# Optimization experiments

Measured on AMD Instinct MI355X. Metric: run time of the kernel, lower is better.

Reference implementation:

```python
import jax, jax.numpy as jnp
import numpy as np
import math

N_EMBD = 1024
N_HEAD = 16
B, T = 2, 2048
MASK_VAL = -10.0  # non-standard soft mask value from original module


def setup_inputs() -> dict:
    key = jax.random.key(0)
    k1, k2, k3 = jax.random.split(key, 3)
    scale = 1.0 / math.sqrt(N_EMBD)
    x = jax.random.normal(k1, (B, T, N_EMBD), dtype=jnp.float32)
    # torch Linear weights: (out_features, in_features)
    w_attn = jax.random.normal(k2, (3 * N_EMBD, N_EMBD), dtype=jnp.float32) * scale
    w_proj = jax.random.normal(k3, (N_EMBD, N_EMBD), dtype=jnp.float32) * scale
    return {"x": x, "w_attn": w_attn, "w_proj": w_proj}


def reference(x, w_attn, w_proj):
    Bsz, Tlen, C = x.shape
    hs = C // N_HEAD
    qkv = jnp.einsum('btc,fc->btf', x, w_attn)  # [B,T,3C]
    q, k, v = jnp.split(qkv, 3, axis=-1)
    # [B,H,T,hs]
    q = q.reshape(Bsz, Tlen, N_HEAD, hs).transpose(0, 2, 1, 3)
    k = k.reshape(Bsz, Tlen, N_HEAD, hs).transpose(0, 2, 1, 3)
    v = v.reshape(Bsz, Tlen, N_HEAD, hs).transpose(0, 2, 1, 3)
    att = jnp.einsum('bhqd,bhkd->bhqk', q, k) * (1.0 / math.sqrt(hs))
    causal = jnp.tril(jnp.ones((Tlen, Tlen), dtype=bool))
    att = jnp.where(causal[None, None], att, MASK_VAL)
    att = jax.nn.softmax(att, axis=-1)
    y = jnp.einsum('bhqk,bhkd->bhqd', att, v)
    y = y.transpose(0, 2, 1, 3).reshape(Bsz, Tlen, C)
    return jnp.einsum('btc,fc->btf', y, w_proj)
```

## Files before the change

### kernel.cpp

```cpp
#include <hip/hip_runtime.h>
#include <hip/hip_bf16.h>
#include <stdint.h>

#define BSZ   2
#define TT    2048
#define NH    16
#define HS    64
#define CC    1024
#define C3    3072
#define MT    4096
#define E10   4.5399929762484854e-05f
#define SCL2  0.1803368801111204f

typedef __bf16 bf16;
typedef __bf16 bf16x8 __attribute__((ext_vector_type(8)));
typedef float  f32x4  __attribute__((ext_vector_type(4)));
typedef short  s16x4  __attribute__((ext_vector_type(4)));

#define AS1 __attribute__((address_space(1)))
#define AS3 __attribute__((address_space(3)))

__device__ __forceinline__ void glds16(const bf16* g, bf16* l) {
    __builtin_amdgcn_global_load_lds((const AS1 void*)g, (AS3 void*)l, 16, 0, 0);
}

__global__ void detect_dtype(const uint16_t* __restrict__ x, int* __restrict__ flag) {
    __shared__ int cnt;
    if (threadIdx.x == 0) cnt = 0;
    __syncthreads();
    int local = 0;
    for (int i = threadIdx.x; i < 512; i += 256) {
        uint16_t u = x[i];
        int e = (u >> 7) & 0xFF;
        if (e >= 96 && e <= 159) local++;
    }
    atomicAdd(&cnt, local);
    __syncthreads();
    if (threadIdx.x == 0) *flag = (cnt >= 461) ? 0 : 1;
}

#define NX8  (MT * CC / 8)
#define NWA8 (C3 * CC / 8)
#define NWP8 (CC * CC / 8)
__global__ __launch_bounds__(256)
void convert_all(const float* __restrict__ x, const float* __restrict__ wa,
                 const float* __restrict__ wp, bf16* __restrict__ xd,
                 bf16* __restrict__ wad, bf16* __restrict__ wpd,
                 const int* __restrict__ flag) {
    if (*flag == 0) return;
    long i = (long)blockIdx.x * 256 + threadIdx.x;
    const float* s; bf16* d; long off;
    if (i < NX8)             { s = x;  d = xd;  off = i; }
    else if (i < NX8 + NWA8) { s = wa; d = wad; off = i - NX8; }
    else                     { s = wp; d = wpd; off = i - NX8 - NWA8; }
    const float4* sp = reinterpret_cast<const float4*>(s) + off * 2;
    float4 a = sp[0], b = sp[1];
    bf16x8 r;
    r[0] = (bf16)a.x; r[1] = (bf16)a.y; r[2] = (bf16)a.z; r[3] = (bf16)a.w;
    r[4] = (bf16)b.x; r[5] = (bf16)b.y; r[6] = (bf16)b.z; r[7] = (bf16)b.w;
    reinterpret_cast<bf16x8*>(d)[off] = r;
}

__global__ __launch_bounds__(256)
void gemm_bt(const bf16* __restrict__ A0, const bf16* __restrict__ A1,
             const bf16* __restrict__ B0, const bf16* __restrict__ B1,
             void* __restrict__ Cmain, bf16* __restrict__ Cv,
             const int* __restrict__ flag,
             int M, int N, int K, int lda, int ldb, int ldc,
             int split_col, int cf32_dyn) {
    __shared__ bf16 As[2][128 * 32];
    __shared__ bf16 Bs[2][128 * 32];

    const int f = *flag;
    const bf16* A = f ? A1 : A0;
    const bf16* B = f ? B1 : B0;
    const int cf32 = cf32_dyn & f;

    const int tid  = threadIdx.x;
    const int lane = tid & 63;
    const int wave = tid >> 6;
    const int wm   = wave >> 1;
    const int wn   = wave & 1;
    const int quad = lane >> 4;
    const int l16  = lane & 15;

    const int row0 = blockIdx.y * 128;
    const int col0 = blockIdx.x * 128;

    const int srow = tid >> 2;
    const int skk  = (tid & 3) * 8;

    const bf16* Ap = A + (long)(row0 + srow) * lda + skk;
    const bf16* Bp = B + (long)(col0 + srow) * ldb + skk;

    auto stage = [&](int k0, int buf) {
        glds16(Ap + k0,                  &As[buf][wave * 512]);
        glds16(Ap + (long)64 * lda + k0, &As[buf][wave * 512 + 2048]);
        glds16(Bp + k0,                  &Bs[buf][wave * 512]);
        glds16(Bp + (long)64 * ldb + k0, &Bs[buf][wave * 512 + 2048]);
    };

    f32x4 acc[4][4] = {};
    stage(0, 0);

    for (int k0 = 0; k0 < K; k0 += 32) {
        const int buf = (k0 >> 5) & 1;
        __syncthreads();
        if (k0 + 32 < K) stage(k0 + 32, buf ^ 1);

        const bf16* Ac = As[buf];
        const bf16* Bc = Bs[buf];
        bf16x8 af[4], bfv[4];
#pragma unroll
        for (int mi = 0; mi < 4; ++mi)
            af[mi] = *reinterpret_cast<const bf16x8*>(&Ac[(wm * 64 + mi * 16 + l16) * 32 + quad * 8]);
#pragma unroll
        for (int ni = 0; ni < 4; ++ni)
            bfv[ni] = *reinterpret_cast<const bf16x8*>(&Bc[(wn * 64 + ni * 16 + l16) * 32 + quad * 8]);
#pragma unroll
        for (int mi = 0; mi < 4; ++mi)
#pragma unroll
            for (int ni = 0; ni < 4; ++ni)
                acc[mi][ni] = __builtin_amdgcn_mfma_f32_16x16x32_bf16(af[mi], bfv[ni], acc[mi][ni], 0, 0, 0);
    }

    if (split_col < 0 || col0 < split_col) {
#pragma unroll
        for (int mi = 0; mi < 4; ++mi)
#pragma unroll
            for (int ni = 0; ni < 4; ++ni)
#pragma unroll
                for (int r = 0; r < 4; ++r) {
                    int row = row0 + wm * 64 + mi * 16 + quad * 4 + r;
                    int col = col0 + wn * 64 + ni * 16 + l16;
                    float v = acc[mi][ni][r];
                    if (cf32) ((float*)Cmain)[(long)row * ldc + col] = v;
                    else      ((bf16*)Cmain)[(long)row * ldc + col] = (bf16)v;
                }
    } else {
        const int h  = (col0 - split_col + wn * 64) >> 6;
        const int bq = row0 >> 11;
        const int tc = ((row0 & 2047) >> 6) + wm;
#pragma unroll
        for (int ni = 0; ni < 4; ++ni) {
            long vrow = (long)(bq * NH + h) * 64 + ni * 16 + l16;
#pragma unroll
            for (int mi = 0; mi < 4; ++mi) {
                bf16 outv[4];
#pragma unroll
                for (int r = 0; r < 4; ++r) outv[r] = (bf16)acc[mi][ni][r];
                *reinterpret_cast<uint2*>(&Cv[vrow * 2048 + tc * 64 + quad * 16 + mi * 4]) =
                    *reinterpret_cast<uint2*>(outv);
            }
        }
    }
}

__global__ __launch_bounds__(256)
void gemm_bt64(const bf16* __restrict__ A0, const bf16* __restrict__ A1,
               const bf16* __restrict__ B0, const bf16* __restrict__ B1,
               void* __restrict__ C, const int* __restrict__ flag,
               int M, int N, int K, int lda, int ldb, int ldc, int cf32_dyn) {
    __shared__ bf16 As[2][128 * 32];
    __shared__ bf16 Bs[2][64 * 32];

    const int f = *flag;
    const bf16* A = f ? A1 : A0;
    const bf16* B = f ? B1 : B0;
    const int cf32 = cf32_dyn & f;

    const int tid  = threadIdx.x;
    const int lane = tid & 63;
    const int wave = tid >> 6;
    const int wm   = wave >> 1;
    const int wn   = wave & 1;
    const int quad = lane >> 4;
    const int l16  = lane & 15;

    const int row0 = blockIdx.y * 128;
    const int col0 = blockIdx.x * 64;

    const int srow = tid >> 2;
    const int skk  = (tid & 3) * 8;

    const bf16* Ap = A + (long)(row0 + srow) * lda + skk;
    const bf16* Bp = B + (long)(col0 + srow) * ldb + skk;

    auto stage = [&](int k0, int buf) {
        glds16(Ap + k0,                  &As[buf][wave * 512]);
        glds16(Ap + (long)64 * lda + k0, &As[buf][wave * 512 + 2048]);
        glds16(Bp + k0,                  &Bs[buf][wave * 512]);
    };

    f32x4 acc[4][2] = {};
    stage(0, 0);

    for (int k0 = 0; k0 < K; k0 += 32) {
        const int buf = (k0 >> 5) & 1;
        __syncthreads();
        if (k0 + 32 < K) stage(k0 + 32, buf ^ 1);

        const bf16* Ac = As[buf];
        const bf16* Bc = Bs[buf];
        bf16x8 af[4], bfv[2];
#pragma unroll
        for (int mi = 0; mi < 4; ++mi)
            af[mi] = *reinterpret_cast<const bf16x8*>(&Ac[(wm * 64 + mi * 16 + l16) * 32 + quad * 8]);
#pragma unroll
        for (int ni = 0; ni < 2; ++ni)
            bfv[ni] = *reinterpret_cast<const bf16x8*>(&Bc[(wn * 32 + ni * 16 + l16) * 32 + quad * 8]);
#pragma unroll
        for (int mi = 0; mi < 4; ++mi)
#pragma unroll
            for (int ni = 0; ni < 2; ++ni)
                acc[mi][ni] = __builtin_amdgcn_mfma_f32_16x16x32_bf16(af[mi], bfv[ni], acc[mi][ni], 0, 0, 0);
    }

#pragma unroll
    for (int mi = 0; mi < 4; ++mi)
#pragma unroll
        for (int ni = 0; ni < 2; ++ni)
#pragma unroll
            for (int r = 0; r < 4; ++r) {
                int row = row0 + wm * 64 + mi * 16 + quad * 4 + r;
                int col = col0 + wn * 32 + ni * 16 + l16;
                float v = acc[mi][ni][r];
                if (cf32) ((float*)C)[(long)row * ldc + col] = v;
                else      ((bf16*)C)[(long)row * ldc + col] = (bf16)v;
            }
}

__global__ __launch_bounds__(256)
void vtile2(const bf16* __restrict__ Vt, float* __restrict__ Vtile) {
    const int kt = blockIdx.x, bh = blockIdx.y;
    const int tid = threadIdx.x;
    const int d = tid >> 2, part = tid & 3;
    const bf16* p = Vt + ((long)bh * 64 + d) * 2048 + kt * 64 + part * 16;
    float s = 0.f;
#pragma unroll
    for (int i = 0; i < 2; ++i) {
        bf16x8 v = *reinterpret_cast<const bf16x8*>(p + i * 8);
#pragma unroll
        for (int j = 0; j < 8; ++j) s += (float)v[j];
    }
    s += __shfl_xor(s, 1, 64);
    s += __shfl_xor(s, 2, 64);
    if (part == 0) Vtile[((long)bh * 32 + kt) * 64 + d] = s;
}

__global__ void vts_suffix(const float* __restrict__ Vtile, float* __restrict__ Vts) {
    const int bh = blockIdx.x, d = threadIdx.x;
    Vts[((long)bh * 33 + 32) * 64 + d] = 0.f;
    float acc = 0.f;
    for (int kt = 31; kt >= 0; --kt) {
        acc += Vtile[((long)bh * 32 + kt) * 64 + d];
        Vts[((long)bh * 33 + kt) * 64 + d] = acc;
    }
}

__global__ __launch_bounds__(256, 3)
void attn(bf16* __restrict__ qk, const bf16* __restrict__ Vt,
          const float* __restrict__ Vts) {
    __shared__ bf16 Ks[3][64 * 64];
    __shared__ bf16 Vs[3][64 * 64];

    const int tid  = threadIdx.x;
    const int lane = tid & 63;
    const int wave = tid >> 6;
    const int quad = lane >> 4;
    const int l16  = lane & 15;

    const int f2   = blockIdx.x;
    const int xcd  = f2 & 7;
    const int slot = f2 >> 3;
    const int u    = slot & 3;
    const int chunk = 31 - (slot >> 2);
    const int h = xcd * 2 + (u & 1);
    const int b = u >> 1;
    const int bh = b * 16 + h;
    const int q0 = chunk * 64;
    const long rbase = (long)b * TT;
    const int ktend = chunk + 1;

    const bf16* qp = qk + (rbase + q0 + wave * 16 + l16) * 2048 + h * HS;
    bf16x8 qf0 = *reinterpret_cast<const bf16x8*>(qp + quad * 8);
    bf16x8 qf1 = *reinterpret_cast<const bf16x8*>(qp + 32 + quad * 8);

    f32x4 O[4] = {};
    float lp = 0.f;

    const int rl  = lane >> 3;
    const int cs  = (lane & 7) ^ rl;
    const int row0dma = wave * 16 + rl;
    const bf16* kgb = qk + (rbase + row0dma) * 2048 + CC + h * HS + cs * 8;
    const bf16* vgb = Vt + ((long)(b * NH + h) * 64 + row0dma) * 2048 + cs * 8;
    const int sx = l16 & 7;

    auto stage = [&](int kt, int buf) {
        glds16(kgb + (long)(kt * 64) * 2048,     &Ks[buf][wave * 1024]);
        glds16(kgb + (long)(kt * 64 + 8) * 2048, &Ks[buf][wave * 1024 + 512]);
        glds16(vgb + kt * 64,                    &Vs[buf][wave * 1024]);
        glds16(vgb + 8 * 2048 + kt * 64,         &Vs[buf][wave * 1024 + 512]);
    };

    stage(0, 0);
    stage(ktend > 1 ? 1 : 0, 1);

    int rb = 0;
    int sb = 2;
    for (int kt = 0; kt < ktend; ++kt) {
        asm volatile("s_waitcnt vmcnt(4)" ::: "memory");
        __builtin_amdgcn_s_barrier();
        __builtin_amdgcn_sched_barrier(0);

        int nkt = kt + 2; nkt = (nkt < ktend) ? nkt : (ktend - 1);
        stage(nkt, sb);

        const bf16* Kc = Ks[rb];
        const bf16* Vc = Vs[rb];

        bf16x8 kf0[4], kf1[4];
#pragma unroll
        for (int g = 0; g < 4; ++g) {
            const int krow = g * 16 + l16;
            kf0[g] = *reinterpret_cast<const bf16x8*>(&Kc[krow * 64 + ((quad ^ sx) * 8)]);
            kf1[g] = *reinterpret_cast<const bf16x8*>(&Kc[krow * 64 + (((4 + quad) ^ sx) * 8)]);
        }
        s16x4 vf[4][4];
#pragma unroll
        for (int dg = 0; dg < 4; ++dg) {
            const int vrow = dg * 16 + l16;
            union { uint4 u; s16x4 s[2]; } ua, ub;
            ua.u = *reinterpret_cast<const uint4*>(&Vc[vrow * 64 + (((2 * quad) ^ sx) * 8)]);
            ub.u = *reinterpret_cast<const uint4*>(&Vc[vrow * 64 + (((2 * quad + 1) ^ sx) * 8)]);
            vf[dg][0] = ua.s[0]; vf[dg][1] = ua.s[1];
            vf[dg][2] = ub.s[0]; vf[dg][3] = ub.s[1];
        }

        f32x4 S[4] = {};
        __builtin_amdgcn_s_setprio(1);
#pragma unroll
        for (int g = 0; g < 4; ++g) {
            S[g] = __builtin_amdgcn_mfma_f32_16x16x32_bf16(kf0[g], qf0, S[g], 0, 0, 0);
            S[g] = __builtin_amdgcn_mfma_f32_16x16x32_bf16(kf1[g], qf1, S[g], 0, 0, 0);
        }
        __builtin_amdgcn_s_setprio(0);

        const bool dtile = (kt == ktend - 1);
        const int ql = wave * 16 + l16;
        s16x4 pk[4];
#pragma unroll
        for (int g = 0; g < 4; ++g) {
#pragma unroll
            for (int r = 0; r < 4; ++r) {
                float p = __builtin_exp2f(S[g][r] * SCL2);
                if (dtile) {
                    int kl = g * 16 + quad * 4 + r;
                    p = (kl > ql) ? E10 : p;
                }
                lp += p;
                union { bf16 b_; short s_; } u2;
                u2.b_ = (bf16)p;
                pk[g][r] = u2.s_;
            }
        }

        __builtin_amdgcn_s_setprio(1);
#pragma unroll
        for (int dg = 0; dg < 4; ++dg) {
            O[dg] = __builtin_amdgcn_mfma_f32_16x16x16bf16_1k(vf[dg][0], pk[0], O[dg], 0, 0, 0);
            O[dg] = __builtin_amdgcn_mfma_f32_16x16x16bf16_1k(vf[dg][1], pk[1], O[dg], 0, 0, 0);
            O[dg] = __builtin_amdgcn_mfma_f32_16x16x16bf16_1k(vf[dg][2], pk[2], O[dg], 0, 0, 0);
            O[dg] = __builtin_amdgcn_mfma_f32_16x16x16bf16_1k(vf[dg][3], pk[3], O[dg], 0, 0, 0);
        }
        __builtin_amdgcn_s_setprio(0);

        rb = (rb == 2) ? 0 : rb + 1;
        sb = (sb == 2) ? 0 : sb + 1;
    }

    lp += __shfl_xor(lp, 16, 64);
    lp += __shfl_xor(lp, 32, 64);

    const int nfut = TT - ktend * 64;
    const float l = lp + (float)nfut * E10;
    const float invl = 1.0f / l;
    const float* vfp = Vts + ((long)bh * 33 + ktend) * 64;

    bf16* yp = qk + (rbase + q0 + wave * 16 + l16) * 2048 + h * HS;
#pragma unroll
    for (int dg = 0; dg < 4; ++dg) {
        bf16 outv[4];
#pragma unroll
        for (int r = 0; r < 4; ++r) {
            float o = O[dg][r] + E10 * vfp[dg * 16 + quad * 4 + r];
            outv[r] = (bf16)(o * invl);
        }
        *reinterpret_cast<uint2*>(yp + dg * 16 + quad * 4) =
            *reinterpret_cast<uint2*>(outv);
    }
}

extern "C" void kernel_launch(void* const* d_in, const int* in_sizes, int n_in,
                              void* d_out, int out_size, void* d_ws, size_t ws_size,
                              hipStream_t stream) {
    const void* x      = d_in[0];
    const void* w_attn = d_in[1];
    const void* w_proj = d_in[2];

    char* ws = (char*)d_ws;
    bf16*  qk     = (bf16*)ws;
    bf16*  Vt     = (bf16*)(ws + (size_t)MT * 2048 * 2);
    char*  p2     = ws + (size_t)MT * 2048 * 2 + (size_t)32 * 64 * 2048 * 2;
    int*   flag   = (int*)p2;
    float* Vts    = (float*)(p2 + 256);
    bf16*  wp_cvt = (bf16*)(p2 + 256 + 32 * 33 * 64 * 4);
    float* Vtile  = (float*)((char*)wp_cvt + (size_t)CC * CC * 2);

    bf16* x_cvt  = (bf16*)d_out;
    bf16* wa_cvt = (bf16*)d_out + (size_t)MT * CC;

    detect_dtype<<<1, 256, 0, stream>>>((const uint16_t*)x, flag);
    convert_all<<<(NX8 + NWA8 + NWP8) / 256, 256, 0, stream>>>(
        (const float*)x, (const float*)w_attn, (const float*)w_proj,
        x_cvt, wa_cvt, wp_cvt, flag);

    gemm_bt<<<dim3(C3 / 128, MT / 128), 256, 0, stream>>>(
        (const bf16*)x, x_cvt, (const bf16*)w_attn, wa_cvt, qk, Vt, flag,
        MT, C3, CC, CC, CC, 2048, 2048, 0);

    vtile2<<<dim3(32, BSZ * NH), 256, 0, stream>>>(Vt, Vtile);
    vts_suffix<<<dim3(BSZ * NH), dim3(64), 0, stream>>>(Vtile, Vts);

    attn<<<dim3(1024), 256, 0, stream>>>(qk, Vt, Vts);

    gemm_bt64<<<dim3(CC / 64, MT / 128), 256, 0, stream>>>(
        qk, qk, (const bf16*)w_proj, wp_cvt, d_out, flag,
        MT, CC, CC, 2048, CC, CC, 1);
}
```

Measured before the change: 185.7 us.

## Fuse dtype detection and V tile sums; software-pipeline attention QK over tiles

Dtype detection moves into every block of the convert kernel, which removes one launch. The per-tile V column sums are now computed in the QKV GEMM epilogue rather than in a separate vtile2 kernel. The attention loop is restructured so the QK^T MFMA and V fragment loads for the next tile are issued before the softmax and PV work of the current tile. These changes cut launch overhead and an extra pass over Vt, and try to overlap MFMA with exp work. In exchange, register pressure in the attention kernel rises and every convert block does redundant detection reads.

```diff
diff --git a/kernel.cpp b/kernel.cpp
--- a/kernel.cpp
+++ b/kernel.cpp
@@ -24,21 +24,6 @@
     __builtin_amdgcn_global_load_lds((const AS1 void*)g, (AS3 void*)l, 16, 0, 0);
 }
 
-__global__ void detect_dtype(const uint16_t* __restrict__ x, int* __restrict__ flag) {
-    __shared__ int cnt;
-    if (threadIdx.x == 0) cnt = 0;
-    __syncthreads();
-    int local = 0;
-    for (int i = threadIdx.x; i < 512; i += 256) {
-        uint16_t u = x[i];
-        int e = (u >> 7) & 0xFF;
-        if (e >= 96 && e <= 159) local++;
-    }
-    atomicAdd(&cnt, local);
-    __syncthreads();
-    if (threadIdx.x == 0) *flag = (cnt >= 461) ? 0 : 1;
-}
-
 #define NX8  (MT * CC / 8)
 #define NWA8 (C3 * CC / 8)
 #define NWP8 (CC * CC / 8)
@@ -46,9 +31,31 @@
 void convert_all(const float* __restrict__ x, const float* __restrict__ wa,
                  const float* __restrict__ wp, bf16* __restrict__ xd,
                  bf16* __restrict__ wad, bf16* __restrict__ wpd,
-                 const int* __restrict__ flag) {
-    if (*flag == 0) return;
-    long i = (long)blockIdx.x * 256 + threadIdx.x;
+                 int* __restrict__ flag) {
+    __shared__ int wsum[4];
+    const int tid = threadIdx.x;
+    const uint16_t* x16 = (const uint16_t*)x;
+    int local = 0;
+    {
+        uint16_t u = x16[tid];
+        int e = (u >> 7) & 0xFF; local += (e >= 96 && e <= 159);
+        u = x16[tid + 256];
+        e = (u >> 7) & 0xFF; local += (e >= 96 && e <= 159);
+    }
+    local += __shfl_xor(local, 1, 64);
+    local += __shfl_xor(local, 2, 64);
+    local += __shfl_xor(local, 4, 64);
+    local += __shfl_xor(local, 8, 64);
+    local += __shfl_xor(local, 16, 64);
+    local += __shfl_xor(local, 32, 64);
+    if ((tid & 63) == 0) wsum[tid >> 6] = local;
+    __syncthreads();
+    const int cnt = wsum[0] + wsum[1] + wsum[2] + wsum[3];
+    const int f = (cnt >= 461) ? 0 : 1;
+    if (blockIdx.x == 0 && tid == 0) *flag = f;
+    if (f == 0) return;
+
+    long i = (long)blockIdx.x * 256 + tid;
     const float* s; bf16* d; long off;
     if (i < NX8)             { s = x;  d = xd;  off = i; }
     else if (i < NX8 + NWA8) { s = wa; d = wad; off = i - NX8; }
@@ -65,6 +72,7 @@
 void gemm_bt(const bf16* __restrict__ A0, const bf16* __restrict__ A1,
              const bf16* __restrict__ B0, const bf16* __restrict__ B1,
              void* __restrict__ Cmain, bf16* __restrict__ Cv,
+             float* __restrict__ Vtile,
              const int* __restrict__ flag,
              int M, int N, int K, int lda, int ldb, int ldc,
              int split_col, int cf32_dyn) {
@@ -153,6 +161,18 @@
                     *reinterpret_cast<uint2*>(outv);
             }
         }
+#pragma unroll
+        for (int ni = 0; ni < 4; ++ni) {
+            float s = 0.f;
+#pragma unroll
+            for (int mi = 0; mi < 4; ++mi)
+#pragma unroll
+                for (int r = 0; r < 4; ++r) s += acc[mi][ni][r];
+            s += __shfl_xor(s, 16, 64);
+            s += __shfl_xor(s, 32, 64);
+            if (quad == 0)
+                Vtile[((long)(bq * NH + h) * 32 + tc) * 64 + ni * 16 + l16] = s;
+        }
     }
 }
 
@@ -228,24 +248,6 @@
                 if (cf32) ((float*)C)[(long)row * ldc + col] = v;
                 else      ((bf16*)C)[(long)row * ldc + col] = (bf16)v;
             }
-}
-
-__global__ __launch_bounds__(256)
-void vtile2(const bf16* __restrict__ Vt, float* __restrict__ Vtile) {
-    const int kt = blockIdx.x, bh = blockIdx.y;
-    const int tid = threadIdx.x;
-    const int d = tid >> 2, part = tid & 3;
-    const bf16* p = Vt + ((long)bh * 64 + d) * 2048 + kt * 64 + part * 16;
-    float s = 0.f;
-#pragma unroll
-    for (int i = 0; i < 2; ++i) {
-        bf16x8 v = *reinterpret_cast<const bf16x8*>(p + i * 8);
-#pragma unroll
-        for (int j = 0; j < 8; ++j) s += (float)v[j];
-    }
-    s += __shfl_xor(s, 1, 64);
-    s += __shfl_xor(s, 2, 64);
-    if (part == 0) Vtile[((long)bh * 32 + kt) * 64 + d] = s;
 }
 
 __global__ void vts_suffix(const float* __restrict__ Vtile, float* __restrict__ Vts) {
@@ -296,29 +298,15 @@
     const bf16* vgb = Vt + ((long)(b * NH + h) * 64 + row0dma) * 2048 + cs * 8;
     const int sx = l16 & 7;
 
-    auto stage = [&](int kt, int buf) {
-        glds16(kgb + (long)(kt * 64) * 2048,     &Ks[buf][wave * 1024]);
-        glds16(kgb + (long)(kt * 64 + 8) * 2048, &Ks[buf][wave * 1024 + 512]);
-        glds16(vgb + kt * 64,                    &Vs[buf][wave * 1024]);
-        glds16(vgb + 8 * 2048 + kt * 64,         &Vs[buf][wave * 1024 + 512]);
+    auto stage = [&](int kt, int bi) {
+        glds16(kgb + (long)(kt * 64) * 2048,     &Ks[bi][wave * 1024]);
+        glds16(kgb + (long)(kt * 64 + 8) * 2048, &Ks[bi][wave * 1024 + 512]);
+        glds16(vgb + kt * 64,                    &Vs[bi][wave * 1024]);
+        glds16(vgb + 8 * 2048 + kt * 64,         &Vs[bi][wave * 1024 + 512]);
     };
 
-    stage(0, 0);
-    stage(ktend > 1 ? 1 : 0, 1);
-
-    int rb = 0;
-    int sb = 2;
-    for (int kt = 0; kt < ktend; ++kt) {
-        asm volatile("s_waitcnt vmcnt(4)" ::: "memory");
-        __builtin_amdgcn_s_barrier();
-        __builtin_amdgcn_sched_barrier(0);
-
-        int nkt = kt + 2; nkt = (nkt < ktend) ? nkt : (ktend - 1);
-        stage(nkt, sb);
-
-        const bf16* Kc = Ks[rb];
-        const bf16* Vc = Vs[rb];
-
+    auto qkTile = [&](int bi, f32x4* Sn) {
+        const bf16* Kc = Ks[bi];
         bf16x8 kf0[4], kf1[4];
 #pragma unroll
         for (int g = 0; g < 4; ++g) {
@@ -326,25 +314,53 @@
             kf0[g] = *reinterpret_cast<const bf16x8*>(&Kc[krow * 64 + ((quad ^ sx) * 8)]);
             kf1[g] = *reinterpret_cast<const bf16x8*>(&Kc[krow * 64 + (((4 + quad) ^ sx) * 8)]);
         }
-        s16x4 vf[4][4];
+        __builtin_amdgcn_s_setprio(1);
+#pragma unroll
+        for (int g = 0; g < 4; ++g) {
+            Sn[g] = __builtin_amdgcn_mfma_f32_16x16x32_bf16(kf0[g], qf0, Sn[g], 0, 0, 0);
+            Sn[g] = __builtin_amdgcn_mfma_f32_16x16x32_bf16(kf1[g], qf1, Sn[g], 0, 0, 0);
+        }
+        __builtin_amdgcn_s_setprio(0);
+    };
+    auto vTile = [&](int bi, s16x4 vf[4][4]) {
+        const bf16* Vc = Vs[bi];
 #pragma unroll
         for (int dg = 0; dg < 4; ++dg) {
             const int vrow = dg * 16 + l16;
-            union { uint4 u; s16x4 s[2]; } ua, ub;
-            ua.u = *reinterpret_cast<const uint4*>(&Vc[vrow * 64 + (((2 * quad) ^ sx) * 8)]);
-            ub.u = *reinterpret_cast<const uint4*>(&Vc[vrow * 64 + (((2 * quad + 1) ^ sx) * 8)]);
+            union { uint4 u4; s16x4 s[2]; } ua, ub;
+            ua.u4 = *reinterpret_cast<const uint4*>(&Vc[vrow * 64 + (((2 * quad) ^ sx) * 8)]);
+            ub.u4 = *reinterpret_cast<const uint4*>(&Vc[vrow * 64 + (((2 * quad + 1) ^ sx) * 8)]);
             vf[dg][0] = ua.s[0]; vf[dg][1] = ua.s[1];
             vf[dg][2] = ub.s[0]; vf[dg][3] = ub.s[1];
         }
-
-        f32x4 S[4] = {};
-        __builtin_amdgcn_s_setprio(1);
-#pragma unroll
-        for (int g = 0; g < 4; ++g) {
-            S[g] = __builtin_amdgcn_mfma_f32_16x16x32_bf16(kf0[g], qf0, S[g], 0, 0, 0);
-            S[g] = __builtin_amdgcn_mfma_f32_16x16x32_bf16(kf1[g], qf1, S[g], 0, 0, 0);
-        }
-        __builtin_amdgcn_s_setprio(0);
+    };
+
+    stage(0, 0);
+    stage(ktend > 1 ? 1 : 0, 1);
+    asm volatile("s_waitcnt vmcnt(4)" ::: "memory");
+    __builtin_amdgcn_s_barrier();
+    __builtin_amdgcn_sched_barrier(0);
+
+    f32x4 Sc[4] = {};
+    s16x4 vc[4][4] = {};
+    qkTile(0, Sc);
+    vTile(0, vc);
+
+    int rb = 1;
+    int sb = 2;
+    for (int kt = 0; kt < ktend; ++kt) {
+        int nkt = kt + 2; nkt = (nkt < ktend) ? nkt : (ktend - 1);
+        stage(nkt, sb);
+        asm volatile("s_waitcnt vmcnt(4)" ::: "memory");
+        __builtin_amdgcn_s_barrier();
+        __builtin_amdgcn_sched_barrier(0);
+
+        f32x4 Sn[4] = {};
+        s16x4 vn[4][4] = {};
+        if (kt + 1 < ktend) {
+            qkTile(rb, Sn);
+            vTile(rb, vn);
+        }
 
         const bool dtile = (kt == ktend - 1);
         const int ql = wave * 16 + l16;
@@ -353,7 +369,7 @@
         for (int g = 0; g < 4; ++g) {
 #pragma unroll
             for (int r = 0; r < 4; ++r) {
-                float p = __builtin_exp2f(S[g][r] * SCL2);
+                float p = __builtin_exp2f(Sc[g][r] * SCL2);
                 if (dtile) {
                     int kl = g * 16 + quad * 4 + r;
                     p = (kl > ql) ? E10 : p;
@@ -368,12 +384,19 @@
         __builtin_amdgcn_s_setprio(1);
 #pragma unroll
         for (int dg = 0; dg < 4; ++dg) {
-            O[dg] = __builtin_amdgcn_mfma_f32_16x16x16bf16_1k(vf[dg][0], pk[0], O[dg], 0, 0, 0);
-            O[dg] = __builtin_amdgcn_mfma_f32_16x16x16bf16_1k(vf[dg][1], pk[1], O[dg], 0, 0, 0);
-            O[dg] = __builtin_amdgcn_mfma_f32_16x16x16bf16_1k(vf[dg][2], pk[2], O[dg], 0, 0, 0);
-            O[dg] = __builtin_amdgcn_mfma_f32_16x16x16bf16_1k(vf[dg][3], pk[3], O[dg], 0, 0, 0);
+            O[dg] = __builtin_amdgcn_mfma_f32_16x16x16bf16_1k(vc[dg][0], pk[0], O[dg], 0, 0, 0);
+            O[dg] = __builtin_amdgcn_mfma_f32_16x16x16bf16_1k(vc[dg][1], pk[1], O[dg], 0, 0, 0);
+            O[dg] = __builtin_amdgcn_mfma_f32_16x16x16bf16_1k(vc[dg][2], pk[2], O[dg], 0, 0, 0);
+            O[dg] = __builtin_amdgcn_mfma_f32_16x16x16bf16_1k(vc[dg][3], pk[3], O[dg], 0, 0, 0);
         }
         __builtin_amdgcn_s_setprio(0);
+
+#pragma unroll
+        for (int g = 0; g < 4; ++g) Sc[g] = Sn[g];
+#pragma unroll
+        for (int dg = 0; dg < 4; ++dg)
+#pragma unroll
+            for (int j = 0; j < 4; ++j) vc[dg][j] = vn[dg][j];
 
         rb = (rb == 2) ? 0 : rb + 1;
         sb = (sb == 2) ? 0 : sb + 1;
@@ -420,16 +443,14 @@
     bf16* x_cvt  = (bf16*)d_out;
     bf16* wa_cvt = (bf16*)d_out + (size_t)MT * CC;
 
-    detect_dtype<<<1, 256, 0, stream>>>((const uint16_t*)x, flag);
     convert_all<<<(NX8 + NWA8 + NWP8) / 256, 256, 0, stream>>>(
         (const float*)x, (const float*)w_attn, (const float*)w_proj,
         x_cvt, wa_cvt, wp_cvt, flag);
 
     gemm_bt<<<dim3(C3 / 128, MT / 128), 256, 0, stream>>>(
-        (const bf16*)x, x_cvt, (const bf16*)w_attn, wa_cvt, qk, Vt, flag,
+        (const bf16*)x, x_cvt, (const bf16*)w_attn, wa_cvt, qk, Vt, Vtile, flag,
         MT, C3, CC, CC, CC, 2048, 2048, 0);
 
-    vtile2<<<dim3(32, BSZ * NH), 256, 0, stream>>>(Vt, Vtile);
     vts_suffix<<<dim3(BSZ * NH), dim3(64), 0, stream>>>(Vtile, Vts);
 
     attn<<<dim3(1024), 256, 0, stream>>>(qk, Vt, Vts);
```

Result: faster. 177.9 us (-4.2%).
